# Kernel optimization log

Measured on AMD Instinct MI355X. Metric: run time of the kernel, lower is better.

Reference implementation:

```python
import jax, jax.numpy as jnp
import numpy as np

B, L, D, H = 4, 4096, 2048, 16
HD = D // H  # head_dim = 128
EPS = 1e-9

def phi(x):
    # ELU(x) + 1 : non-negative feature map
    return jax.nn.elu(x) + 1.0

def setup_inputs() -> dict:
    key = jax.random.key(0)
    k1, k2, k3 = jax.random.split(key, 3)
    x = jax.random.normal(k1, (B, L, D), dtype=jnp.float32)
    W_qkv = jax.random.normal(k2, (3 * D, D), dtype=jnp.float32) * (D ** -0.5)
    W_out = jax.random.normal(k3, (D, D), dtype=jnp.float32) * (D ** -0.5)
    return {"x": x, "W_qkv": W_qkv, "W_out": W_out}

def reference(x, W_qkv, W_out):
    b, l, d = x.shape
    qkv = x @ W_qkv.T                      # (B, L, 3D)
    q, k, v = jnp.split(qkv, 3, axis=-1)   # each (B, L, D)
    # (B, L, H, HD) -> (B, H, L, HD)
    q = q.reshape(b, l, H, HD).transpose(0, 2, 1, 3)
    k = k.reshape(b, l, H, HD).transpose(0, 2, 1, 3)
    v = v.reshape(b, l, H, HD).transpose(0, 2, 1, 3)
    q = phi(q)
    k = phi(k)
    kv_cumsum = jnp.cumsum(k * v, axis=2)  # prefix sum over sequence dim
    k_cumsum = jnp.cumsum(k, axis=2)
    out = q * kv_cumsum / (q * k_cumsum + EPS)
    out = out.transpose(0, 2, 1, 3).reshape(b, l, d)
    return (out @ W_out.T) * (HD ** -0.5)
```

## Files before the change

kernel.cpp:

```cpp
#include <hip/hip_runtime.h>
#include <hip/hip_bf16.h>
#include <stdint.h>

#define B_ 4
#define L_ 4096
#define D_ 2048
#define TD_ (3 * D_)
#define CHUNKS 128
#define CLEN (L_ / CHUNKS)
#define M_ (B_ * L_)
#define K_ 2048
#define NT (K_ / 64)

typedef __bf16 bf16x8 __attribute__((ext_vector_type(8)));
typedef float f32x4 __attribute__((ext_vector_type(4)));
typedef ushort u16x8 __attribute__((ext_vector_type(8)));

__device__ __forceinline__ ushort f2bf(float f) {
  uint32_t u = __builtin_bit_cast(uint32_t, f);
  u += 0x7fffu + ((u >> 16) & 1u);
  return (ushort)(u >> 16);
}

__device__ __forceinline__ float bf2f(ushort u) {
  return __builtin_bit_cast(float, (uint32_t)u << 16);
}

__device__ __forceinline__ float phi_f(float x) {
  return x > 0.f ? x + 1.f : __expf(x);
}

__device__ __forceinline__ void gload_lds16(const ushort* g, ushort* l) {
  __builtin_amdgcn_global_load_lds(
      (__attribute__((address_space(1))) void*)(g),
      (__attribute__((address_space(3))) void*)(l), 16, 0, 0);
}

#define SBAR() __builtin_amdgcn_s_barrier()
#define SCHED0() __builtin_amdgcn_sched_barrier(0)
#define LGKM0() asm volatile("s_waitcnt lgkmcnt(0)" ::: "memory")
#define MFMA16(a, b, c) __builtin_amdgcn_mfma_f32_16x16x32_bf16((a), (b), (c), 0, 0, 0)

__global__ void cvt_bf16_kernel(const float* __restrict__ in,
                                ushort* __restrict__ out, int n4) {
  int i = blockIdx.x * blockDim.x + threadIdx.x;
  if (i >= n4) return;
  float4 v = reinterpret_cast<const float4*>(in)[i];
  ushort4 o;
  o.x = f2bf(v.x); o.y = f2bf(v.y); o.z = f2bf(v.z); o.w = f2bf(v.w);
  reinterpret_cast<ushort4*>(out)[i] = o;
}

__device__ __forceinline__ void stage_half(const ushort* __restrict__ G,
                                           int row0, int k0, char* lds_half,
                                           int tid) {
#pragma unroll
  for (int lp = 0; lp < 2; ++lp) {
    const int p = lp * 8192 + tid * 16;
    const int row = p >> 7;
    const int cb = (p & 127) ^ ((row & 7) << 4);
    gload_lds16(G + (size_t)(row0 + row) * K_ + k0 + (cb >> 1),
                (ushort*)(lds_half + p));
  }
}

#define RD(p, off) (*reinterpret_cast<const bf16x8*>((p) + (off)))

#define KTILE(t, c)                                                            \
  {                                                                            \
    const int P = (c) * 32768;                                                 \
                 \
    _Pragma("unroll") for (int i = 0; i < 4; ++i) {                            \
      af[i][0] = RD(bA0, P + i * 2048);                                        \
      af[i][1] = RD(bA1, P + i * 2048);                                        \
    }                                                                          \
    _Pragma("unroll") for (int j = 0; j < 2; ++j) {                            \
      bfr[j][0] = RD(bB0, P + j * 2048);                                       \
      bfr[j][1] = RD(bB1, P + j * 2048);                                       \
    }                                                                          \
    if ((t) + 1 < NT) stage_half(A, rA, (t) * 64 + 64, lsA + (P ^ 32768), tid);\
    SCHED0(); SBAR(); LGKM0(); SCHED0();                                       \
    __builtin_amdgcn_s_setprio(1);                                             \
    _Pragma("unroll") for (int i = 0; i < 4; ++i)                              \
    _Pragma("unroll") for (int j = 0; j < 2; ++j)                              \
    _Pragma("unroll") for (int ks = 0; ks < 2; ++ks)                           \
        acc[i][j] = MFMA16(af[i][ks], bfr[j][ks], acc[i][j]);                  \
    __builtin_amdgcn_s_setprio(0); SBAR();                                     \
                          \
    _Pragma("unroll") for (int j = 2; j < 4; ++j) {                            \
      bfr[j][0] = RD(bB0, P + j * 2048);                                       \
      bfr[j][1] = RD(bB1, P + j * 2048);                                       \
    }                                                                          \
    if ((t) + 1 < NT)                                                          \
      stage_half(A, rA + 128, (t) * 64 + 64, lsA + (P ^ 32768) + 16384, tid);  \
    SCHED0(); SBAR(); LGKM0(); SCHED0();                                       \
    __builtin_amdgcn_s_setprio(1);                                             \
    _Pragma("unroll") for (int i = 0; i < 4; ++i)                              \
    _Pragma("unroll") for (int j = 2; j < 4; ++j)                              \
    _Pragma("unroll") for (int ks = 0; ks < 2; ++ks)                           \
        acc[i][j] = MFMA16(af[i][ks], bfr[j][ks], acc[i][j]);                  \
    __builtin_amdgcn_s_setprio(0); SBAR();                                     \
                     \
    _Pragma("unroll") for (int i = 0; i < 4; ++i) {                            \
      af[i][0] = RD(bA0, P + 8192 + i * 2048);                                 \
      af[i][1] = RD(bA1, P + 8192 + i * 2048);                                 \
    }                                                                          \
    if ((t) + 2 < NT) stage_half(Bm, rB, (t) * 64 + 128, lsB + P, tid);        \
    SCHED0(); SBAR(); LGKM0(); SCHED0();                                       \
    __builtin_amdgcn_s_setprio(1);                                             \
    _Pragma("unroll") for (int i = 0; i < 4; ++i)                              \
    _Pragma("unroll") for (int j = 2; j < 4; ++j)                              \
    _Pragma("unroll") for (int ks = 0; ks < 2; ++ks)                           \
        acc[4 + i][j] = MFMA16(af[i][ks], bfr[j][ks], acc[4 + i][j]);          \
    __builtin_amdgcn_s_setprio(0); SBAR();                                     \
                  \
    if ((t) + 2 < NT) {                                                        \
      stage_half(Bm, rB + 128, (t) * 64 + 128, lsB + P + 16384, tid);          \
      SCHED0();                                                                \
      asm volatile("s_waitcnt vmcnt(4)" ::: "memory");                         \
    } else {                                                                   \
      SCHED0();                                                                \
      asm volatile("s_waitcnt vmcnt(0)" ::: "memory");                         \
    }                                                                          \
    SBAR();                                                                    \
    __builtin_amdgcn_s_setprio(1);                                             \
    _Pragma("unroll") for (int i = 0; i < 4; ++i)                              \
    _Pragma("unroll") for (int j = 0; j < 2; ++j)                              \
    _Pragma("unroll") for (int ks = 0; ks < 2; ++ks)                           \
        acc[4 + i][j] = MFMA16(af[i][ks], bfr[j][ks], acc[4 + i][j]);          \
    __builtin_amdgcn_s_setprio(0); SBAR();                                     \
  }

__device__ __forceinline__ void gemm_core(const ushort* __restrict__ A,
                                          const ushort* __restrict__ Bm,
                                          int bm, int bn, char* ls,
                                          f32x4 (&acc)[8][4]) {
  const int tid = threadIdx.x;
  const int lane = tid & 63, wid = tid >> 6;
  const int wm = (wid >> 2) * 128, wn = (wid & 3) * 64;
  const int l16 = lane & 15, kg = lane >> 4;
  const int rA = bm * 256, rB = bn * 256;

  char* lsA = ls;
  char* lsB = ls + 65536;

  const int v16 = (l16 & 7) << 4;
  const int c0 = (kg * 16) ^ v16;
  const int c1 = (64 + kg * 16) ^ v16;
  const char* bA0 = lsA + (wm + l16) * 128 + c0;
  const char* bA1 = lsA + (wm + l16) * 128 + c1;
  const char* bB0 = lsB + (wn + l16) * 128 + c0;
  const char* bB1 = lsB + (wn + l16) * 128 + c1;

  stage_half(A, rA, 0, lsA, tid);
  stage_half(A, rA + 128, 0, lsA + 16384, tid);
  stage_half(Bm, rB, 0, lsB, tid);
  stage_half(Bm, rB + 128, 0, lsB + 16384, tid);
  stage_half(Bm, rB, 64, lsB + 32768, tid);
  stage_half(Bm, rB + 128, 64, lsB + 32768 + 16384, tid);
  asm volatile("s_waitcnt vmcnt(4)" ::: "memory");
  SBAR();

  bf16x8 af[4][2], bfr[4][2];
#pragma unroll 1
  for (int t2 = 0; t2 < NT; t2 += 2) {
    KTILE(t2, 0);
    KTILE(t2 + 1, 1);
  }
}

__global__ __launch_bounds__(512, 2) void gemm_qkv8(
    const ushort* __restrict__ A, const ushort* __restrict__ Bm,
    ushort* __restrict__ qb, ushort* __restrict__ kb, ushort* __restrict__ vb) {
  extern __shared__ char ls[];
  const int nwg = gridDim.x;
  const int wg = blockIdx.x;
  const int swz = (wg & 7) * (nwg >> 3) + (wg >> 3);
  const int MT = M_ / 256;
  const int bm = swz % MT, bn = swz / MT;

  f32x4 acc[8][4] = {};
  gemm_core(A, Bm, bm, bn, ls, acc);

  const int seg = bn >> 3;
  ushort* dst = seg == 0 ? qb : (seg == 1 ? kb : vb);
  const int colbase = bn * 256 - seg * 2048;
  const int tid = threadIdx.x;
  const int lane = tid & 63, wid = tid >> 6;
  const int wm = (wid >> 2) * 128, wn = (wid & 3) * 64;
  const int l16 = lane & 15, kg = lane >> 4;
#pragma unroll
  for (int i = 0; i < 8; ++i) {
    const int row0 = bm * 256 + wm + i * 16 + kg * 4;
#pragma unroll
    for (int j = 0; j < 4; ++j) {
      const int col = colbase + wn + j * 16 + l16;
      ushort* cp = dst + (size_t)row0 * D_ + col;
#pragma unroll
      for (int r = 0; r < 4; ++r) cp[(size_t)r * D_] = f2bf(acc[i][j][r]);
    }
  }
}

__global__ __launch_bounds__(512, 2) void gemm_out8(
    const ushort* __restrict__ A, const ushort* __restrict__ Bm,
    float* __restrict__ C, float scale) {
  extern __shared__ char ls[];
  const int nwg = gridDim.x;
  const int wg = blockIdx.x;
  const int swz = (wg & 7) * (nwg >> 3) + (wg >> 3);
  const int MT = M_ / 256;
  const int bm = swz % MT, bn = swz / MT;

  f32x4 acc[8][4] = {};
  gemm_core(A, Bm, bm, bn, ls, acc);

  const int tid = threadIdx.x;
  const int lane = tid & 63, wid = tid >> 6;
  const int wm = (wid >> 2) * 128, wn = (wid & 3) * 64;
  const int l16 = lane & 15, kg = lane >> 4;
#pragma unroll
  for (int i = 0; i < 8; ++i) {
    const int row0 = bm * 256 + wm + i * 16 + kg * 4;
#pragma unroll
    for (int j = 0; j < 4; ++j) {
      const int col = bn * 256 + wn + j * 16 + l16;
      float* cp = C + (size_t)row0 * D_ + col;
#pragma unroll
      for (int r = 0; r < 4; ++r) cp[(size_t)r * D_] = acc[i][j][r] * scale;
    }
  }
}

__global__ void chunk_sums_kernel(const ushort* __restrict__ kb,
                                  const ushort* __restrict__ vb,
                                  float* __restrict__ sums) {
  const int d0 = threadIdx.x * 8;
  const int b = blockIdx.y, c = blockIdx.z;
  float sk[8] = {}, skv[8] = {};
  const size_t rowbase = (size_t)b * L_ + (size_t)c * CLEN;
  for (int l = 0; l < CLEN; ++l) {
    const size_t idx = (rowbase + l) * D_ + d0;
    u16x8 k8 = *reinterpret_cast<const u16x8*>(kb + idx);
    u16x8 v8 = *reinterpret_cast<const u16x8*>(vb + idx);
#pragma unroll
    for (int j = 0; j < 8; ++j) {
      float k = phi_f(bf2f(k8[j]));
      sk[j] += k;
      skv[j] = fmaf(k, bf2f(v8[j]), skv[j]);
    }
  }
  float* s = sums + ((size_t)(b * CHUNKS + c) * 2) * D_ + d0;
#pragma unroll
  for (int j = 0; j < 8; ++j) {
    s[j] = sk[j];
    s[D_ + j] = skv[j];
  }
}

__global__ void chunk_prefix_kernel(float* __restrict__ sums) {
  const int idx = blockIdx.x * 256 + threadIdx.x;
  const int b = idx >> 11, d = idx & (D_ - 1);
  float rk = 0.f, rkv = 0.f;
  for (int c = 0; c < CHUNKS; ++c) {
    float* s = sums + ((size_t)(b * CHUNKS + c) * 2) * D_ + d;
    float sk = s[0], skv = s[D_];
    s[0] = rk;
    s[D_] = rkv;
    rk += sk;
    rkv += skv;
  }
}

__global__ void apply_kernel(const ushort* __restrict__ qb,
                             const ushort* __restrict__ kb,
                             const ushort* __restrict__ vb,
                             const float* __restrict__ sums,
                             ushort* __restrict__ outb) {
  const int d0 = threadIdx.x * 8;
  const int b = blockIdx.y, c = blockIdx.z;
  const float* s = sums + ((size_t)(b * CHUNKS + c) * 2) * D_ + d0;
  float rk[8], rkv[8];
#pragma unroll
  for (int j = 0; j < 8; ++j) {
    rk[j] = s[j];
    rkv[j] = s[D_ + j];
  }
  const size_t rowbase = (size_t)b * L_ + (size_t)c * CLEN;
  for (int l = 0; l < CLEN; ++l) {
    const size_t idx = (rowbase + l) * D_ + d0;
    u16x8 q8 = *reinterpret_cast<const u16x8*>(qb + idx);
    u16x8 k8 = *reinterpret_cast<const u16x8*>(kb + idx);
    u16x8 v8 = *reinterpret_cast<const u16x8*>(vb + idx);
    u16x8 o8;
#pragma unroll
    for (int j = 0; j < 8; ++j) {
      float q = phi_f(bf2f(q8[j]));
      float k = phi_f(bf2f(k8[j]));
      float v = bf2f(v8[j]);
      rkv[j] = fmaf(k, v, rkv[j]);
      rk[j] += k;
      float o = (q * rkv[j]) / fmaf(q, rk[j], 1e-9f);
      o8[j] = f2bf(o);
    }
    *reinterpret_cast<u16x8*>(outb + idx) = o8;
  }
}

extern "C" void kernel_launch(void* const* d_in, const int* in_sizes, int n_in,
                              void* d_out, int out_size, void* d_ws, size_t ws_size,
                              hipStream_t stream) {
  (void)in_sizes; (void)n_in; (void)out_size; (void)ws_size;
  const float* x = (const float*)d_in[0];
  const float* Wqkv = (const float*)d_in[1];
  const float* Wout = (const float*)d_in[2];
  float* out = (float*)d_out;

  ushort* kb = (ushort*)d_out;
  ushort* vb = kb + (size_t)M_ * D_;

  char* ws = (char*)d_ws;
  size_t off = 0;
  auto alloc = [&](size_t bytes) -> void* {
    off = (off + 255) & ~(size_t)255;
    void* p = ws + off;
    off += bytes;
    return p;
  };
  ushort* qb = (ushort*)alloc((size_t)M_ * D_ * 2);
  ushort* xb = (ushort*)alloc((size_t)M_ * D_ * 2);
  ushort* wqb = (ushort*)alloc((size_t)TD_ * D_ * 2);
  ushort* wob = (ushort*)alloc((size_t)D_ * D_ * 2);
  float* sums = (float*)alloc((size_t)B_ * CHUNKS * 2 * D_ * 4);
  ushort* outb = xb;

  (void)hipFuncSetAttribute((const void*)gemm_qkv8,
                            hipFuncAttributeMaxDynamicSharedMemorySize, 131072);
  (void)hipFuncSetAttribute((const void*)gemm_out8,
                            hipFuncAttributeMaxDynamicSharedMemorySize, 131072);

  cvt_bf16_kernel<<<(M_ * D_ / 4 + 255) / 256, 256, 0, stream>>>(x, xb, M_ * D_ / 4);
  cvt_bf16_kernel<<<(TD_ * D_ / 4 + 255) / 256, 256, 0, stream>>>(Wqkv, wqb, TD_ * D_ / 4);
  cvt_bf16_kernel<<<(D_ * D_ / 4 + 255) / 256, 256, 0, stream>>>(Wout, wob, D_ * D_ / 4);

  gemm_qkv8<<<dim3((TD_ / 256) * (M_ / 256)), 512, 131072, stream>>>(xb, wqb, qb, kb, vb);

  chunk_sums_kernel<<<dim3(1, B_, CHUNKS), 256, 0, stream>>>(kb, vb, sums);
  chunk_prefix_kernel<<<dim3(B_ * D_ / 256), 256, 0, stream>>>(sums);
  apply_kernel<<<dim3(1, B_, CHUNKS), 256, 0, stream>>>(qb, kb, vb, sums, outb);

  gemm_out8<<<dim3((D_ / 256) * (M_ / 256)), 512, 131072, stream>>>(outb, wob, out,
                                                                    0.08838834764831845f);
}
```

Measured before the change: 620.2 us.

## Shrink GEMM M tile to 128 and restructure LDS pipeline with register double-buffering

Both GEMMs now use a 128x256 block tile instead of 256x256, which halves the accumulators per wave and cuts LDS to 96KB. The k-loop is rewritten to prefetch the next tile's LDS fragments into a second register set, with fewer barriers and partial lgkmcnt waits. The aim is higher occupancy and less barrier overhead, at the cost of lower arithmetic intensity per block and more global traffic for the B operand.

```diff
diff --git a/kernel.cpp b/kernel.cpp
--- a/kernel.cpp
+++ b/kernel.cpp
@@ -38,7 +38,6 @@
 
 #define SBAR() __builtin_amdgcn_s_barrier()
 #define SCHED0() __builtin_amdgcn_sched_barrier(0)
-#define LGKM0() asm volatile("s_waitcnt lgkmcnt(0)" ::: "memory")
 #define MFMA16(a, b, c) __builtin_amdgcn_mfma_f32_16x16x32_bf16((a), (b), (c), 0, 0, 0)
 
 __global__ void cvt_bf16_kernel(const float* __restrict__ in,
@@ -51,71 +50,46 @@
   reinterpret_cast<ushort4*>(out)[i] = o;
 }
 
-__device__ __forceinline__ void stage_half(const ushort* __restrict__ G,
-                                           int row0, int k0, char* lds_half,
-                                           int tid) {
-#pragma unroll
-  for (int lp = 0; lp < 2; ++lp) {
-    const int p = lp * 8192 + tid * 16;
-    const int row = p >> 7;
-    const int cb = (p & 127) ^ ((row & 7) << 4);
-    gload_lds16(G + (size_t)(row0 + row) * K_ + k0 + (cb >> 1),
-                (ushort*)(lds_half + p));
-  }
+__device__ __forceinline__ void stage8k(const ushort* __restrict__ G,
+                                        int row0, int k0, char* lds8k,
+                                        int tid) {
+  const int p = tid * 16;
+  const int row = tid >> 3;
+  const int cb = (p & 127) ^ ((row & 7) << 4);
+  gload_lds16(G + (size_t)(row0 + row) * K_ + k0 + (cb >> 1),
+              (ushort*)(lds8k + p));
 }
 
 #define RD(p, off) (*reinterpret_cast<const bf16x8*>((p) + (off)))
 
 #define KTILE(t, c)                                                            \
   {                                                                            \
-    const int P = (c) * 32768;                                                 \
-                 \
-    _Pragma("unroll") for (int i = 0; i < 4; ++i) {                            \
-      af[i][0] = RD(bA0, P + i * 2048);                                        \
-      af[i][1] = RD(bA1, P + i * 2048);                                        \
+                                                             \
+    _Pragma("unroll") for (int i = 0; i < 4; ++i)                              \
+        af1[i] = RD(bA1, (c) * 16384 + i * 2048);                              \
+    _Pragma("unroll") for (int j = 0; j < 4; ++j)                              \
+        bf1[j] = RD(bB1, (c) * 32768 + j * 2048);                              \
+    if ((t) + 1 < NT) {                                                        \
+      stage8k(A, rA, (t) * 64 + 64, lsA + (1 - (c)) * 16384, tid);             \
+      stage8k(A, rA + 64, (t) * 64 + 64, lsA + (1 - (c)) * 16384 + 8192, tid); \
     }                                                                          \
-    _Pragma("unroll") for (int j = 0; j < 2; ++j) {                            \
-      bfr[j][0] = RD(bB0, P + j * 2048);                                       \
-      bfr[j][1] = RD(bB1, P + j * 2048);                                       \
-    }                                                                          \
-    if ((t) + 1 < NT) stage_half(A, rA, (t) * 64 + 64, lsA + (P ^ 32768), tid);\
-    SCHED0(); SBAR(); LGKM0(); SCHED0();                                       \
+    SCHED0();                                                                  \
+    asm volatile("s_waitcnt lgkmcnt(8)" ::: "memory");                         \
+    SCHED0();                                                                  \
     __builtin_amdgcn_s_setprio(1);                                             \
     _Pragma("unroll") for (int i = 0; i < 4; ++i)                              \
-    _Pragma("unroll") for (int j = 0; j < 2; ++j)                              \
-    _Pragma("unroll") for (int ks = 0; ks < 2; ++ks)                           \
-        acc[i][j] = MFMA16(af[i][ks], bfr[j][ks], acc[i][j]);                  \
-    __builtin_amdgcn_s_setprio(0); SBAR();                                     \
-                          \
-    _Pragma("unroll") for (int j = 2; j < 4; ++j) {                            \
-      bfr[j][0] = RD(bB0, P + j * 2048);                                       \
-      bfr[j][1] = RD(bB1, P + j * 2048);                                       \
-    }                                                                          \
-    if ((t) + 1 < NT)                                                          \
-      stage_half(A, rA + 128, (t) * 64 + 64, lsA + (P ^ 32768) + 16384, tid);  \
-    SCHED0(); SBAR(); LGKM0(); SCHED0();                                       \
-    __builtin_amdgcn_s_setprio(1);                                             \
-    _Pragma("unroll") for (int i = 0; i < 4; ++i)                              \
-    _Pragma("unroll") for (int j = 2; j < 4; ++j)                              \
-    _Pragma("unroll") for (int ks = 0; ks < 2; ++ks)                           \
-        acc[i][j] = MFMA16(af[i][ks], bfr[j][ks], acc[i][j]);                  \
-    __builtin_amdgcn_s_setprio(0); SBAR();                                     \
-                     \
-    _Pragma("unroll") for (int i = 0; i < 4; ++i) {                            \
-      af[i][0] = RD(bA0, P + 8192 + i * 2048);                                 \
-      af[i][1] = RD(bA1, P + 8192 + i * 2048);                                 \
-    }                                                                          \
-    if ((t) + 2 < NT) stage_half(Bm, rB, (t) * 64 + 128, lsB + P, tid);        \
-    SCHED0(); SBAR(); LGKM0(); SCHED0();                                       \
-    __builtin_amdgcn_s_setprio(1);                                             \
-    _Pragma("unroll") for (int i = 0; i < 4; ++i)                              \
-    _Pragma("unroll") for (int j = 2; j < 4; ++j)                              \
-    _Pragma("unroll") for (int ks = 0; ks < 2; ++ks)                           \
-        acc[4 + i][j] = MFMA16(af[i][ks], bfr[j][ks], acc[4 + i][j]);          \
-    __builtin_amdgcn_s_setprio(0); SBAR();                                     \
-                  \
+    _Pragma("unroll") for (int j = 0; j < 4; ++j)                              \
+        acc[i][j] = MFMA16(af0[i], bf0[j], acc[i][j]);                         \
+    __builtin_amdgcn_s_setprio(0);                                             \
+                                                             \
+    asm volatile("s_waitcnt lgkmcnt(0)" ::: "memory");                         \
+    SCHED0();                                                                  \
+    SBAR();                                                                    \
     if ((t) + 2 < NT) {                                                        \
-      stage_half(Bm, rB + 128, (t) * 64 + 128, lsB + P + 16384, tid);          \
+      stage8k(Bm, rB, (t) * 64 + 128, lsB + (c) * 32768, tid);                 \
+      stage8k(Bm, rB + 64, (t) * 64 + 128, lsB + (c) * 32768 + 8192, tid);     \
+      stage8k(Bm, rB + 128, (t) * 64 + 128, lsB + (c) * 32768 + 16384, tid);   \
+      stage8k(Bm, rB + 192, (t) * 64 + 128, lsB + (c) * 32768 + 24576, tid);   \
       SCHED0();                                                                \
       asm volatile("s_waitcnt vmcnt(4)" ::: "memory");                         \
     } else {                                                                   \
@@ -123,26 +97,32 @@
       asm volatile("s_waitcnt vmcnt(0)" ::: "memory");                         \
     }                                                                          \
     SBAR();                                                                    \
+    if ((t) + 1 < NT) {                                                        \
+      _Pragma("unroll") for (int i = 0; i < 4; ++i)                            \
+          af0[i] = RD(bA0, (1 - (c)) * 16384 + i * 2048);                      \
+      _Pragma("unroll") for (int j = 0; j < 4; ++j)                            \
+          bf0[j] = RD(bB0, (1 - (c)) * 32768 + j * 2048);                      \
+    }                                                                          \
+    SCHED0();                                                                  \
     __builtin_amdgcn_s_setprio(1);                                             \
     _Pragma("unroll") for (int i = 0; i < 4; ++i)                              \
-    _Pragma("unroll") for (int j = 0; j < 2; ++j)                              \
-    _Pragma("unroll") for (int ks = 0; ks < 2; ++ks)                           \
-        acc[4 + i][j] = MFMA16(af[i][ks], bfr[j][ks], acc[4 + i][j]);          \
-    __builtin_amdgcn_s_setprio(0); SBAR();                                     \
+    _Pragma("unroll") for (int j = 0; j < 4; ++j)                              \
+        acc[i][j] = MFMA16(af1[i], bf1[j], acc[i][j]);                         \
+    __builtin_amdgcn_s_setprio(0);                                             \
   }
 
 __device__ __forceinline__ void gemm_core(const ushort* __restrict__ A,
                                           const ushort* __restrict__ Bm,
                                           int bm, int bn, char* ls,
-                                          f32x4 (&acc)[8][4]) {
+                                          f32x4 (&acc)[4][4]) {
   const int tid = threadIdx.x;
   const int lane = tid & 63, wid = tid >> 6;
-  const int wm = (wid >> 2) * 128, wn = (wid & 3) * 64;
+  const int wm = (wid >> 2) * 64, wn = (wid & 3) * 64;
   const int l16 = lane & 15, kg = lane >> 4;
-  const int rA = bm * 256, rB = bn * 256;
+  const int rA = bm * 128, rB = bn * 256;
 
   char* lsA = ls;
-  char* lsB = ls + 65536;
+  char* lsB = ls + 32768;
 
   const int v16 = (l16 & 7) << 4;
   const int c0 = (kg * 16) ^ v16;
@@ -152,16 +132,25 @@
   const char* bB0 = lsB + (wn + l16) * 128 + c0;
   const char* bB1 = lsB + (wn + l16) * 128 + c1;
 
-  stage_half(A, rA, 0, lsA, tid);
-  stage_half(A, rA + 128, 0, lsA + 16384, tid);
-  stage_half(Bm, rB, 0, lsB, tid);
-  stage_half(Bm, rB + 128, 0, lsB + 16384, tid);
-  stage_half(Bm, rB, 64, lsB + 32768, tid);
-  stage_half(Bm, rB + 128, 64, lsB + 32768 + 16384, tid);
+  stage8k(A, rA, 0, lsA, tid);
+  stage8k(A, rA + 64, 0, lsA + 8192, tid);
+  stage8k(Bm, rB, 0, lsB, tid);
+  stage8k(Bm, rB + 64, 0, lsB + 8192, tid);
+  stage8k(Bm, rB + 128, 0, lsB + 16384, tid);
+  stage8k(Bm, rB + 192, 0, lsB + 24576, tid);
+  stage8k(Bm, rB, 64, lsB + 32768, tid);
+  stage8k(Bm, rB + 64, 64, lsB + 32768 + 8192, tid);
+  stage8k(Bm, rB + 128, 64, lsB + 32768 + 16384, tid);
+  stage8k(Bm, rB + 192, 64, lsB + 32768 + 24576, tid);
   asm volatile("s_waitcnt vmcnt(4)" ::: "memory");
   SBAR();
 
-  bf16x8 af[4][2], bfr[4][2];
+  bf16x8 af0[4], af1[4], bf0[4], bf1[4];
+#pragma unroll
+  for (int i = 0; i < 4; ++i) af0[i] = RD(bA0, i * 2048);
+#pragma unroll
+  for (int j = 0; j < 4; ++j) bf0[j] = RD(bB0, j * 2048);
+
 #pragma unroll 1
   for (int t2 = 0; t2 < NT; t2 += 2) {
     KTILE(t2, 0);
@@ -176,10 +165,10 @@
   const int nwg = gridDim.x;
   const int wg = blockIdx.x;
   const int swz = (wg & 7) * (nwg >> 3) + (wg >> 3);
-  const int MT = M_ / 256;
+  const int MT = M_ / 128;
   const int bm = swz % MT, bn = swz / MT;
 
-  f32x4 acc[8][4] = {};
+  f32x4 acc[4][4] = {};
   gemm_core(A, Bm, bm, bn, ls, acc);
 
   const int seg = bn >> 3;
@@ -187,11 +176,11 @@
   const int colbase = bn * 256 - seg * 2048;
   const int tid = threadIdx.x;
   const int lane = tid & 63, wid = tid >> 6;
-  const int wm = (wid >> 2) * 128, wn = (wid & 3) * 64;
+  const int wm = (wid >> 2) * 64, wn = (wid & 3) * 64;
   const int l16 = lane & 15, kg = lane >> 4;
 #pragma unroll
-  for (int i = 0; i < 8; ++i) {
-    const int row0 = bm * 256 + wm + i * 16 + kg * 4;
+  for (int i = 0; i < 4; ++i) {
+    const int row0 = bm * 128 + wm + i * 16 + kg * 4;
 #pragma unroll
     for (int j = 0; j < 4; ++j) {
       const int col = colbase + wn + j * 16 + l16;
@@ -209,19 +198,19 @@
   const int nwg = gridDim.x;
   const int wg = blockIdx.x;
   const int swz = (wg & 7) * (nwg >> 3) + (wg >> 3);
-  const int MT = M_ / 256;
+  const int MT = M_ / 128;
   const int bm = swz % MT, bn = swz / MT;
 
-  f32x4 acc[8][4] = {};
+  f32x4 acc[4][4] = {};
   gemm_core(A, Bm, bm, bn, ls, acc);
 
   const int tid = threadIdx.x;
   const int lane = tid & 63, wid = tid >> 6;
-  const int wm = (wid >> 2) * 128, wn = (wid & 3) * 64;
+  const int wm = (wid >> 2) * 64, wn = (wid & 3) * 64;
   const int l16 = lane & 15, kg = lane >> 4;
 #pragma unroll
-  for (int i = 0; i < 8; ++i) {
-    const int row0 = bm * 256 + wm + i * 16 + kg * 4;
+  for (int i = 0; i < 4; ++i) {
+    const int row0 = bm * 128 + wm + i * 16 + kg * 4;
 #pragma unroll
     for (int j = 0; j < 4; ++j) {
       const int col = bn * 256 + wn + j * 16 + l16;
@@ -335,20 +324,20 @@
   ushort* outb = xb;
 
   (void)hipFuncSetAttribute((const void*)gemm_qkv8,
-                            hipFuncAttributeMaxDynamicSharedMemorySize, 131072);
+                            hipFuncAttributeMaxDynamicSharedMemorySize, 98304);
   (void)hipFuncSetAttribute((const void*)gemm_out8,
-                            hipFuncAttributeMaxDynamicSharedMemorySize, 131072);
+                            hipFuncAttributeMaxDynamicSharedMemorySize, 98304);
 
   cvt_bf16_kernel<<<(M_ * D_ / 4 + 255) / 256, 256, 0, stream>>>(x, xb, M_ * D_ / 4);
   cvt_bf16_kernel<<<(TD_ * D_ / 4 + 255) / 256, 256, 0, stream>>>(Wqkv, wqb, TD_ * D_ / 4);
   cvt_bf16_kernel<<<(D_ * D_ / 4 + 255) / 256, 256, 0, stream>>>(Wout, wob, D_ * D_ / 4);
 
-  gemm_qkv8<<<dim3((TD_ / 256) * (M_ / 256)), 512, 131072, stream>>>(xb, wqb, qb, kb, vb);
+  gemm_qkv8<<<dim3((TD_ / 256) * (M_ / 128)), 512, 98304, stream>>>(xb, wqb, qb, kb, vb);
 
   chunk_sums_kernel<<<dim3(1, B_, CHUNKS), 256, 0, stream>>>(kb, vb, sums);
   chunk_prefix_kernel<<<dim3(B_ * D_ / 256), 256, 0, stream>>>(sums);
   apply_kernel<<<dim3(1, B_, CHUNKS), 256, 0, stream>>>(qb, kb, vb, sums, outb);
 
-  gemm_out8<<<dim3((D_ / 256) * (M_ / 256)), 512, 131072, stream>>>(outb, wob, out,
-                                                                    0.08838834764831845f);
-}
+  gemm_out8<<<dim3((D_ / 256) * (M_ / 128)), 512, 98304, stream>>>(outb, wob, out,
+                                                                   0.08838834764831845f);
+}
```

New measurement: 664.8 us. +7.2%, slower.

## Simplify GEMM k-loop to plain double buffering with one barrier per tile

Applied to the files above, without the earlier changes.

Replaces the four-phase interleaved k-tile schedule, which staged A one tile ahead and B two tiles ahead with a barrier around each phase, with a simple double buffer. All A and B loads for the next tile are issued at the top, and the current tile's fragments are read and multiplied. A single vmcnt(0) wait and barrier ends each tile. This removes many barriers and lgkm waits, but the new loads are drained fully every tile and the B prefetch depth drops from two tiles to one, so less memory latency can be hidden.

```diff
diff --git a/kernel.cpp b/kernel.cpp
--- a/kernel.cpp
+++ b/kernel.cpp
@@ -38,7 +38,6 @@
 
 #define SBAR() __builtin_amdgcn_s_barrier()
 #define SCHED0() __builtin_amdgcn_sched_barrier(0)
-#define LGKM0() asm volatile("s_waitcnt lgkmcnt(0)" ::: "memory")
 #define MFMA16(a, b, c) __builtin_amdgcn_mfma_f32_16x16x32_bf16((a), (b), (c), 0, 0, 0)
 
 __global__ void cvt_bf16_kernel(const float* __restrict__ in,
@@ -68,67 +67,42 @@
 
 #define KTILE(t, c)                                                            \
   {                                                                            \
-    const int P = (c) * 32768;                                                 \
-                 \
+    if ((t) + 1 < NT) {                                                        \
+      const int kn = ((t) + 1) * 64;                                           \
+      stage_half(A, rA, kn, lsA + (1 - (c)) * 32768, tid);                     \
+      stage_half(A, rA + 128, kn, lsA + (1 - (c)) * 32768 + 16384, tid);       \
+      stage_half(Bm, rB, kn, lsB + (1 - (c)) * 32768, tid);                    \
+      stage_half(Bm, rB + 128, kn, lsB + (1 - (c)) * 32768 + 16384, tid);      \
+    }                                                                          \
+    SCHED0();                                                                  \
     _Pragma("unroll") for (int i = 0; i < 4; ++i) {                            \
-      af[i][0] = RD(bA0, P + i * 2048);                                        \
-      af[i][1] = RD(bA1, P + i * 2048);                                        \
+      af[i][0] = RD(bA0, (c) * 32768 + i * 2048);                              \
+      af[i][1] = RD(bA1, (c) * 32768 + i * 2048);                              \
     }                                                                          \
-    _Pragma("unroll") for (int j = 0; j < 2; ++j) {                            \
-      bfr[j][0] = RD(bB0, P + j * 2048);                                       \
-      bfr[j][1] = RD(bB1, P + j * 2048);                                       \
+    _Pragma("unroll") for (int j = 0; j < 4; ++j) {                            \
+      bfr[j][0] = RD(bB0, (c) * 32768 + j * 2048);                             \
+      bfr[j][1] = RD(bB1, (c) * 32768 + j * 2048);                             \
     }                                                                          \
-    if ((t) + 1 < NT) stage_half(A, rA, (t) * 64 + 64, lsA + (P ^ 32768), tid);\
-    SCHED0(); SBAR(); LGKM0(); SCHED0();                                       \
     __builtin_amdgcn_s_setprio(1);                                             \
     _Pragma("unroll") for (int i = 0; i < 4; ++i)                              \
-    _Pragma("unroll") for (int j = 0; j < 2; ++j)                              \
+    _Pragma("unroll") for (int j = 0; j < 4; ++j)                              \
     _Pragma("unroll") for (int ks = 0; ks < 2; ++ks)                           \
         acc[i][j] = MFMA16(af[i][ks], bfr[j][ks], acc[i][j]);                  \
-    __builtin_amdgcn_s_setprio(0); SBAR();                                     \
-                          \
-    _Pragma("unroll") for (int j = 2; j < 4; ++j) {                            \
-      bfr[j][0] = RD(bB0, P + j * 2048);                                       \
-      bfr[j][1] = RD(bB1, P + j * 2048);                                       \
+    __builtin_amdgcn_s_setprio(0);                                             \
+    _Pragma("unroll") for (int i = 0; i < 4; ++i) {                            \
+      af[i][0] = RD(bA0, (c) * 32768 + 8192 + i * 2048);                       \
+      af[i][1] = RD(bA1, (c) * 32768 + 8192 + i * 2048);                       \
     }                                                                          \
-    if ((t) + 1 < NT)                                                          \
-      stage_half(A, rA + 128, (t) * 64 + 64, lsA + (P ^ 32768) + 16384, tid);  \
-    SCHED0(); SBAR(); LGKM0(); SCHED0();                                       \
     __builtin_amdgcn_s_setprio(1);                                             \
     _Pragma("unroll") for (int i = 0; i < 4; ++i)                              \
-    _Pragma("unroll") for (int j = 2; j < 4; ++j)                              \
-    _Pragma("unroll") for (int ks = 0; ks < 2; ++ks)                           \
-        acc[i][j] = MFMA16(af[i][ks], bfr[j][ks], acc[i][j]);                  \
-    __builtin_amdgcn_s_setprio(0); SBAR();                                     \
-                     \
-    _Pragma("unroll") for (int i = 0; i < 4; ++i) {                            \
-      af[i][0] = RD(bA0, P + 8192 + i * 2048);                                 \
-      af[i][1] = RD(bA1, P + 8192 + i * 2048);                                 \
-    }                                                                          \
-    if ((t) + 2 < NT) stage_half(Bm, rB, (t) * 64 + 128, lsB + P, tid);        \
-    SCHED0(); SBAR(); LGKM0(); SCHED0();                                       \
-    __builtin_amdgcn_s_setprio(1);                                             \
-    _Pragma("unroll") for (int i = 0; i < 4; ++i)                              \
-    _Pragma("unroll") for (int j = 2; j < 4; ++j)                              \
+    _Pragma("unroll") for (int j = 0; j < 4; ++j)                              \
     _Pragma("unroll") for (int ks = 0; ks < 2; ++ks)                           \
         acc[4 + i][j] = MFMA16(af[i][ks], bfr[j][ks], acc[4 + i][j]);          \
-    __builtin_amdgcn_s_setprio(0); SBAR();                                     \
-                  \
-    if ((t) + 2 < NT) {                                                        \
-      stage_half(Bm, rB + 128, (t) * 64 + 128, lsB + P + 16384, tid);          \
-      SCHED0();                                                                \
-      asm volatile("s_waitcnt vmcnt(4)" ::: "memory");                         \
-    } else {                                                                   \
-      SCHED0();                                                                \
-      asm volatile("s_waitcnt vmcnt(0)" ::: "memory");                         \
-    }                                                                          \
+    __builtin_amdgcn_s_setprio(0);                                             \
+    SCHED0();                                                                  \
+    asm volatile("s_waitcnt vmcnt(0)" ::: "memory");                           \
     SBAR();                                                                    \
-    __builtin_amdgcn_s_setprio(1);                                             \
-    _Pragma("unroll") for (int i = 0; i < 4; ++i)                              \
-    _Pragma("unroll") for (int j = 0; j < 2; ++j)                              \
-    _Pragma("unroll") for (int ks = 0; ks < 2; ++ks)                           \
-        acc[4 + i][j] = MFMA16(af[i][ks], bfr[j][ks], acc[4 + i][j]);          \
-    __builtin_amdgcn_s_setprio(0); SBAR();                                     \
+    SCHED0();                                                                  \
   }
 
 __device__ __forceinline__ void gemm_core(const ushort* __restrict__ A,
@@ -156,10 +130,9 @@
   stage_half(A, rA + 128, 0, lsA + 16384, tid);
   stage_half(Bm, rB, 0, lsB, tid);
   stage_half(Bm, rB + 128, 0, lsB + 16384, tid);
-  stage_half(Bm, rB, 64, lsB + 32768, tid);
-  stage_half(Bm, rB + 128, 64, lsB + 32768 + 16384, tid);
-  asm volatile("s_waitcnt vmcnt(4)" ::: "memory");
+  asm volatile("s_waitcnt vmcnt(0)" ::: "memory");
   SBAR();
+  SCHED0();
 
   bf16x8 af[4][2], bfr[4][2];
 #pragma unroll 1
```

After: 621.2 us (median of 2 runs). No clear change (+0.2%).
